# Kernel tuning notes

Measured on AMD Instinct MI355X. Metric: run time of the kernel, lower is better.

The kernel has to match this reference:

```python
import jax, jax.numpy as jnp
import numpy as np

NUM_HEAD_CHANNELS = 64
GROUPS = 32
EPS = 1e-5


def setup_inputs() -> dict:
    key = jax.random.key(0)
    ks = jax.random.split(key, 3)
    B, C, H, W = 16, 512, 64, 64
    x = jax.random.normal(ks[0], (B, C, H, W), jnp.float32)
    gn_gamma = jnp.ones((C,), jnp.float32)
    gn_beta = jnp.zeros((C,), jnp.float32)
    # 1x1 conv weights (out_ch, in_ch); fan-in scaling keeps softmax logits sane
    w_qkv = jax.random.normal(ks[1], (3 * C, C), jnp.float32) / np.float32(np.sqrt(C))
    b_qkv = jnp.zeros((3 * C,), jnp.float32)
    w_proj = jax.random.normal(ks[2], (C, C), jnp.float32) / np.float32(np.sqrt(C))
    b_proj = jnp.zeros((C,), jnp.float32)
    return dict(x=x, gn_gamma=gn_gamma, gn_beta=gn_beta, w_qkv=w_qkv,
                b_qkv=b_qkv, w_proj=w_proj, b_proj=b_proj)


def _group_norm(x, gamma, beta):
    B, C, H, W = x.shape
    xg = x.reshape(B, GROUPS, C // GROUPS, H, W)
    mu = xg.mean(axis=(2, 3, 4), keepdims=True)
    var = xg.var(axis=(2, 3, 4), keepdims=True)
    xn = ((xg - mu) * jax.lax.rsqrt(var + EPS)).reshape(B, C, H, W)
    return xn * gamma[None, :, None, None] + beta[None, :, None, None]


def reference(x, gn_gamma, gn_beta, w_qkv, b_qkv, w_proj, b_proj):
    B, C, H, W = x.shape
    L = H * W
    heads = C // NUM_HEAD_CHANNELS
    Lh = L // heads  # module splits spatial length across heads

    xn = _group_norm(x, gn_gamma, gn_beta).reshape(B, C, L)
    # 1x1 conv QKV: (3C, C) x (B, C, L) -> (B, 3C, L)
    qkv = jnp.einsum('oc,bcl->bol', w_qkv, xn) + b_qkv[None, :, None]
    qkv = qkv.reshape(B, 3 * C, heads, Lh)
    q, k, v = jnp.split(qkv, 3, axis=1)  # each (B, C, heads, Lh)

    scale = np.float32(1.0 / np.sqrt(C // heads))
    w_att = jnp.einsum('bchq,bchk->bhqk', q * scale, k)  # (B, heads, Lh, Lh)
    w_att = jax.nn.softmax(w_att.astype(jnp.float32), axis=-1).astype(q.dtype)
    a = jnp.einsum('bhqk,bchk->bchq', w_att, v)  # (B, C, heads, Lh)
    a = a.reshape(B, C, L)  # contiguous reinterpretation, as torch .view

    out = jnp.einsum('oc,bcl->bol', w_proj, a) + b_proj[None, :, None]
    return x + out.reshape(B, C, H, W)
```

## Files before the change

kernel.cpp:

```cpp
#include <hip/hip_runtime.h>

typedef unsigned short u16;
typedef __attribute__((ext_vector_type(8))) short bf16x8;
typedef __attribute__((ext_vector_type(4))) short bf16x4;
typedef __attribute__((ext_vector_type(4))) float f32x4;

__device__ __forceinline__ float bf2f(u16 u){ union { unsigned int i; float f; } v; v.i = ((unsigned int)u) << 16; return v.f; }
__device__ __forceinline__ u16 f2bf(float f){ union { float f; unsigned int i; } v; v.f = f; unsigned int r = v.i + 0x7fffu + ((v.i >> 16) & 1u); return (u16)(r >> 16); }

#define MFMA(a,b,c) __builtin_amdgcn_mfma_f32_16x16x32_bf16((a),(b),(c),0,0,0)

__device__ __forceinline__ void gl_lds16(const u16* g, u16* l){
  __builtin_amdgcn_global_load_lds((const __attribute__((address_space(1))) unsigned int*)g,
                                   (__attribute__((address_space(3))) unsigned int*)l, 16, 0, 0);
}

__global__ __launch_bounds__(256) void k_gn_stats(const float* __restrict__ x, float* __restrict__ stats){
  const int bg = blockIdx.x;
  const float4* p = (const float4*)(x + (size_t)bg * 65536);
  const int tid = threadIdx.x;
  float s = 0.f, sq = 0.f;
  for (int i = 0; i < 64; ++i){
    float4 v = p[tid + i*256];
    s += v.x + v.y + v.z + v.w;
    sq += v.x*v.x + v.y*v.y + v.z*v.z + v.w*v.w;
  }
#pragma unroll
  for (int d = 32; d > 0; d >>= 1){ s += __shfl_down(s, d, 64); sq += __shfl_down(sq, d, 64); }
  __shared__ float ls[4], lq[4];
  if ((tid & 63) == 0){ ls[tid>>6] = s; lq[tid>>6] = sq; }
  __syncthreads();
  if (tid == 0){
    float S = ls[0]+ls[1]+ls[2]+ls[3];
    float Q = lq[0]+lq[1]+lq[2]+lq[3];
    float mean = S * (1.f/65536.f);
    float var  = Q * (1.f/65536.f) - mean*mean;
    stats[bg*2]   = mean;
    stats[bg*2+1] = rsqrtf(var + 1e-5f);
  }
}

__global__ __launch_bounds__(256) void k_conv_w(const float* __restrict__ wq, const float* __restrict__ wp,
                                                u16* __restrict__ wout){
  const int base = (blockIdx.x*256 + threadIdx.x) * 4;
  float4 v;
  if (base < 786432) v = *(const float4*)(wq + base);
  else               v = *(const float4*)(wp + (base - 786432));
  bf16x4 o;
  o[0] = (short)f2bf(v.x); o[1] = (short)f2bf(v.y); o[2] = (short)f2bf(v.z); o[3] = (short)f2bf(v.w);
  *(bf16x4*)(wout + base) = o;
}

__global__ __launch_bounds__(256) void k_gn_t(const float* __restrict__ x, const float* __restrict__ stats,
                                              const float* __restrict__ gamma, const float* __restrict__ beta,
                                              u16* __restrict__ xnt){
  __shared__ u16 tile[64*72];
  const int l0 = blockIdx.x*64, c0 = blockIdx.y*64, b = blockIdx.z;
  const int tid = threadIdx.x;
#pragma unroll
  for (int i = 0; i < 2; ++i){
    int v = tid + i*256; int cc = v >> 3, seg = v & 7;
    int c = c0 + cc;
    float mu = stats[(b*32 + (c>>4))*2], rs = stats[(b*32 + (c>>4))*2 + 1];
    float ga = gamma[c] * rs;
    float be = beta[c] - mu * ga;
    const float* px = x + ((size_t)(b*512 + c))*4096 + l0 + seg*8;
    float4 a0 = *(const float4*)px;
    float4 a1 = *(const float4*)(px + 4);
    bf16x8 ov;
    ov[0]=(short)f2bf(a0.x*ga+be); ov[1]=(short)f2bf(a0.y*ga+be);
    ov[2]=(short)f2bf(a0.z*ga+be); ov[3]=(short)f2bf(a0.w*ga+be);
    ov[4]=(short)f2bf(a1.x*ga+be); ov[5]=(short)f2bf(a1.y*ga+be);
    ov[6]=(short)f2bf(a1.z*ga+be); ov[7]=(short)f2bf(a1.w*ga+be);
    *(bf16x8*)&tile[cc*72 + seg*8] = ov;
  }
  __syncthreads();
#pragma unroll
  for (int i = 0; i < 2; ++i){
    int v = tid + i*256; int ll = v >> 3, seg = v & 7;
    bf16x8 ov;
#pragma unroll
    for (int j = 0; j < 8; ++j) ov[j] = (short)tile[(seg*8 + j)*72 + ll];
    *(bf16x8*)(xnt + ((size_t)(b*4096 + l0 + ll))*512 + c0 + seg*8) = ov;
  }
}

__global__ __launch_bounds__(256,2) void k_qkv(const u16* __restrict__ xnt, const u16* __restrict__ wq,
                                               const float* __restrict__ bq,
                                               u16* __restrict__ Qt, u16* __restrict__ Kt, u16* __restrict__ Vh){
  __shared__ u16 smem[17408];
  u16* sA = smem;
  u16* sW = smem + 8192;
  const int l0 = blockIdx.x*128, o0 = blockIdx.y*128, b = blockIdx.z;
  const int tid = threadIdx.x, wv = tid>>6, lane = tid&63, g = lane>>4, r = lane&15;
  const int wm = wv>>1, wn = wv&1;
  const u16* Ab = xnt + ((size_t)(b*4096 + l0))*512;
  const u16* Wb = wq  + (size_t)o0*512;
  int srow[4], scol[4];
#pragma unroll
  for (int j = 0; j < 4; ++j){
    int s = wv*256 + j*64 + lane;
    srow[j] = s >> 3;
    scol[j] = ((s & 7) ^ (srow[j] & 7)) * 8;
  }
  f32x4 acc[4][4];
#pragma unroll
  for (int mt = 0; mt < 4; ++mt)
#pragma unroll
    for (int nt = 0; nt < 4; ++nt) acc[mt][nt] = (f32x4){0.f,0.f,0.f,0.f};

  const int key = r & 7;
  for (int c0 = 0; c0 < 512; c0 += 64){
    __syncthreads();
#pragma unroll
    for (int j = 0; j < 4; ++j){
      u16* ldst = &smem[(wv*256 + j*64)*8];
      gl_lds16(Ab + (size_t)srow[j]*512 + c0 + scol[j], ldst);
      gl_lds16(Wb + (size_t)srow[j]*512 + c0 + scol[j], ldst + 8192);
    }
    __syncthreads();
#pragma unroll
    for (int half = 0; half < 2; ++half){
      bf16x8 a[4], w[4];
#pragma unroll
      for (int mt = 0; mt < 4; ++mt){ int R = wm*64 + mt*16 + r; a[mt] = *(const bf16x8*)&sA[(R*8 + ((half*4+g) ^ key))*8]; }
#pragma unroll
      for (int nt = 0; nt < 4; ++nt){ int R = wn*64 + nt*16 + r; w[nt] = *(const bf16x8*)&sW[(R*8 + ((half*4+g) ^ key))*8]; }
#pragma unroll
      for (int mt = 0; mt < 4; ++mt)
#pragma unroll
        for (int nt = 0; nt < 4; ++nt) acc[mt][nt] = MFMA(a[mt], w[nt], acc[mt][nt]);
    }
  }
  __syncthreads();
  const int t   = blockIdx.y >> 2;
  const int cp0 = (blockIdx.y & 3)*128;
  const int h   = blockIdx.x >> 2;
  const int lh0 = (blockIdx.x & 3)*128;
#pragma unroll
  for (int nt = 0; nt < 4; ++nt){
    const int ol = wn*64 + nt*16 + r;
    const float bi = bq[o0 + ol];
#pragma unroll
    for (int mt = 0; mt < 4; ++mt){
      const int ll = wm*64 + mt*16 + g*4;
      if (t == 2){
        bf16x4 pk;
#pragma unroll
        for (int rr = 0; rr < 4; ++rr) pk[rr] = (short)f2bf(acc[mt][nt][rr] + bi);
        *(bf16x4*)&smem[ol*136 + ll] = pk;
      } else {
#pragma unroll
        for (int rr = 0; rr < 4; ++rr) smem[(ll + rr)*136 + ol] = f2bf(acc[mt][nt][rr] + bi);
      }
    }
  }
  __syncthreads();
  const size_t bh = (size_t)(b*8 + h);
  u16* dst = (t == 0) ? Qt : Kt;
#pragma unroll
  for (int i = 0; i < 8; ++i){
    int v = tid + i*256; int row = v >> 4, seg = v & 15;
    bf16x8 d = *(const bf16x8*)&smem[row*136 + seg*8];
    if (t == 2){
      *(bf16x8*)(Vh + (bh*512 + cp0 + row)*512 + lh0 + seg*8) = d;
    } else {
      *(bf16x8*)(dst + (bh*512 + lh0 + row)*512 + cp0 + seg*8) = d;
    }
  }
}

__global__ __launch_bounds__(512,2) void k_attn(const u16* __restrict__ Qt, const u16* __restrict__ Kt,
                                                const u16* __restrict__ Vh, u16* __restrict__ At){
  extern __shared__ __align__(16) u16 smem[];
  float* sMax = (float*)(smem + 65536);
  float* sSum = sMax + 512;
  const int wgid = blockIdx.x;
  const int orig = (wgid & 7)*64 + (wgid >> 3);
  const int b = orig >> 5, h = (orig >> 2) & 7, q0 = (orig & 3) * 128;
  const int bh = b*8 + h;
  const int tid = threadIdx.x, wv = tid>>6, lane = tid&63, g = lane>>4, r = lane&15;
  const int wq = wv>>2, wk = wv&3;
  const size_t base = (size_t)bh * 262144;
  const u16* Qb = Qt + base + (size_t)q0*512;
  const u16* Kb = Kt + base;
  const u16* Vb = Vh + base;

  const u16* gsrc[5];
  int ldoff[5];
  {
    const int l4 = lane >> 2, pc = lane & 3;
#pragma unroll
    for (int j = 0; j < 5; ++j){
      const int i = wv*5 + j;
      const int row = ((i < 8) ? (i*16) : ((i-8)*16)) + l4;
      const u16* bp = (i < 8) ? (Qb + (size_t)row*512) : (Kb + (size_t)row*512);
      gsrc[j] = bp + ((pc ^ (row & 3)) * 8);
      ldoff[j] = i * 512;
    }
  }

  f32x4 s[4][8];
#pragma unroll
  for (int mt = 0; mt < 4; ++mt)
#pragma unroll
    for (int nt = 0; nt < 8; ++nt) s[mt][nt] = (f32x4){0.f,0.f,0.f,0.f};

  const int qswz = (g ^ (r & 3)) * 8;

#define STAGE_QK(bufbase, c0) do { \
    u16* _bb = (bufbase); \
    _Pragma("unroll") \
    for (int _j = 0; _j < 5; ++_j) gl_lds16(gsrc[_j] + (c0), _bb + ldoff[_j]); \
  } while(0)

#define QK_COMPUTE(bbp) do { \
    const u16* _cb = (bbp); \
    bf16x8 a_[4], kb_[8]; \
    _Pragma("unroll") \
    for (int _mt = 0; _mt < 4; ++_mt) a_[_mt] = *(const bf16x8*)&_cb[(wq*64 + _mt*16 + r)*32 + qswz]; \
    _Pragma("unroll") \
    for (int _nt = 0; _nt < 8; ++_nt) kb_[_nt] = *(const bf16x8*)&_cb[4096 + (wk*128 + _nt*16 + r)*32 + qswz]; \
    __builtin_amdgcn_s_setprio(1); \
    _Pragma("unroll") \
    for (int _mt = 0; _mt < 4; ++_mt) \
      _Pragma("unroll") \
      for (int _nt = 0; _nt < 8; ++_nt) s[_mt][_nt] = MFMA(a_[_mt], kb_[_nt], s[_mt][_nt]); \
    __builtin_amdgcn_s_setprio(0); \
  } while(0)

  STAGE_QK(smem,         0);
  STAGE_QK(smem + 20480, 32);
  int bcur = 0;
  for (int cs = 0; cs < 15; ++cs){
    asm volatile("s_waitcnt vmcnt(5)" ::: "memory");
    __builtin_amdgcn_s_barrier();
    __builtin_amdgcn_sched_barrier(0);
    if (cs < 14){
      int bn = bcur + 2; if (bn >= 3) bn -= 3;
      STAGE_QK(smem + bn*20480, (cs+2)*32);
    }
    QK_COMPUTE(smem + bcur*20480);
    if (++bcur == 3) bcur = 0;
  }
  asm volatile("s_waitcnt vmcnt(0)" ::: "memory");
  __builtin_amdgcn_s_barrier();
  __builtin_amdgcn_sched_barrier(0);
  QK_COMPUTE(smem + bcur*20480);

#pragma unroll
  for (int mt = 0; mt < 4; ++mt)
#pragma unroll
    for (int nt = 0; nt < 8; ++nt)
#pragma unroll
      for (int rr = 0; rr < 4; ++rr) s[mt][nt][rr] *= 0.125f;

  float mx[4][4];
#pragma unroll
  for (int mt = 0; mt < 4; ++mt)
#pragma unroll
    for (int rr = 0; rr < 4; ++rr){
      float m = s[mt][0][rr];
#pragma unroll
      for (int nt = 1; nt < 8; ++nt) m = fmaxf(m, s[mt][nt][rr]);
      m = fmaxf(m, __shfl_xor(m, 1, 64)); m = fmaxf(m, __shfl_xor(m, 2, 64));
      m = fmaxf(m, __shfl_xor(m, 4, 64)); m = fmaxf(m, __shfl_xor(m, 8, 64));
      mx[mt][rr] = m;
    }
  if (r == 0){
#pragma unroll
    for (int mt = 0; mt < 4; ++mt)
#pragma unroll
      for (int rr = 0; rr < 4; ++rr) sMax[(wq*64 + mt*16 + g*4 + rr)*4 + wk] = mx[mt][rr];
  }
  __syncthreads();
#pragma unroll
  for (int mt = 0; mt < 4; ++mt)
#pragma unroll
    for (int rr = 0; rr < 4; ++rr){
      float4 v = *(const float4*)&sMax[(wq*64 + mt*16 + g*4 + rr)*4];
      mx[mt][rr] = fmaxf(fmaxf(v.x, v.y), fmaxf(v.z, v.w));
    }
  float inv[4][4];
#pragma unroll
  for (int mt = 0; mt < 4; ++mt)
#pragma unroll
    for (int rr = 0; rr < 4; ++rr){
      float t = 0.f;
#pragma unroll
      for (int nt = 0; nt < 8; ++nt){
        float e = __expf(s[mt][nt][rr] - mx[mt][rr]);
        s[mt][nt][rr] = e; t += e;
      }
      t += __shfl_xor(t, 1, 64); t += __shfl_xor(t, 2, 64);
      t += __shfl_xor(t, 4, 64); t += __shfl_xor(t, 8, 64);
      inv[mt][rr] = t;
    }
  if (r == 0){
#pragma unroll
    for (int mt = 0; mt < 4; ++mt)
#pragma unroll
      for (int rr = 0; rr < 4; ++rr) sSum[(wq*64 + mt*16 + g*4 + rr)*4 + wk] = inv[mt][rr];
  }
  __syncthreads();
#pragma unroll
  for (int mt = 0; mt < 4; ++mt)
#pragma unroll
    for (int rr = 0; rr < 4; ++rr){
      float4 v = *(const float4*)&sSum[(wq*64 + mt*16 + g*4 + rr)*4];
      inv[mt][rr] = 1.f / (v.x + v.y + v.z + v.w);
    }
  {
    const int kx7 = r & 7, kbase = wk*16 + (r>>3);
#pragma unroll
    for (int mt = 0; mt < 4; ++mt)
#pragma unroll
      for (int rr = 0; rr < 4; ++rr){
        const int q = wq*64 + mt*16 + g*4 + rr;
        const int ro = q*512, qx = q & 7;
        const float iv = inv[mt][rr];
#pragma unroll
        for (int nt = 0; nt < 8; ++nt){
          const int ch = kbase + nt*2;
          smem[ro + ((ch ^ qx) * 8) + kx7] = f2bf(s[mt][nt][rr] * iv);
        }
      }
  }
  const u16* Vw = Vb + (size_t)(wv*64 + r)*512 + g*8;
  bf16x8 vf[2][4];
#pragma unroll
  for (int mt = 0; mt < 4; ++mt) vf[0][mt] = *(const bf16x8*)(Vw + mt*8192);
  __syncthreads();

  f32x4 o[4][8];
#pragma unroll
  for (int mt = 0; mt < 4; ++mt)
#pragma unroll
    for (int nt = 0; nt < 8; ++nt) o[mt][nt] = (f32x4){0.f,0.f,0.f,0.f};
#pragma unroll
  for (int kk = 0; kk < 16; ++kk){
    if (kk < 15){
#pragma unroll
      for (int mt = 0; mt < 4; ++mt) vf[(kk+1)&1][mt] = *(const bf16x8*)(Vw + mt*8192 + (kk+1)*32);
    }
    bf16x8 pp[8];
#pragma unroll
    for (int nt = 0; nt < 8; ++nt){
      const int q = nt*16 + r;
      pp[nt] = *(const bf16x8*)&smem[q*512 + (((kk*4 + g) ^ (r & 7)) * 8)];
    }
    __builtin_amdgcn_s_setprio(1);
#pragma unroll
    for (int mt = 0; mt < 4; ++mt)
#pragma unroll
      for (int nt = 0; nt < 8; ++nt) o[mt][nt] = MFMA(vf[kk&1][mt], pp[nt], o[mt][nt]);
    __builtin_amdgcn_s_setprio(0);
  }
  __syncthreads();

#pragma unroll
  for (int mt = 0; mt < 4; ++mt){
    const int c = wv*64 + mt*16 + g*4;
    const int ch = c >> 3, cl = c & 7;
#pragma unroll
    for (int nt = 0; nt < 8; ++nt){
      const int q = nt*16 + r;
      bf16x4 pk;
#pragma unroll
      for (int rr = 0; rr < 4; ++rr) pk[rr] = (short)f2bf(o[mt][nt][rr]);
      *(bf16x4*)&smem[q*512 + ((ch ^ (r & 7)) * 8) + cl] = pk;
    }
  }
  __syncthreads();
  u16* Ad = At + ((size_t)(bh*512 + q0))*512;
#pragma unroll
  for (int i = 0; i < 16; ++i){
    const int idx = tid + i*512, q = idx >> 6, ch = idx & 63;
    bf16x8 d = *(const bf16x8*)&smem[q*512 + ((ch ^ (q & 7)) * 8)];
    *(bf16x8*)(Ad + (size_t)q*512 + ch*8) = d;
  }
#undef STAGE_QK
#undef QK_COMPUTE
}

__global__ __launch_bounds__(256,2) void k_proj(const u16* __restrict__ At, const u16* __restrict__ wp,
                                                const float* __restrict__ bpr, const float* __restrict__ x,
                                                float* __restrict__ out){
  __shared__ u16 smem[17408];
  u16* sA = smem;
  u16* sW = smem + 8192;
  const int l0 = blockIdx.x*128, o0 = blockIdx.y*128, b = blockIdx.z;
  const int tid = threadIdx.x, wv = tid>>6, lane = tid&63, g = lane>>4, r = lane&15;
  const int wm = wv>>1, wn = wv&1;
  const u16* Ab = At + ((size_t)(b*4096 + l0))*512;
  const u16* Wb = wp + (size_t)o0*512;
  int srow[4], scol[4];
#pragma unroll
  for (int j = 0; j < 4; ++j){
    int s = wv*256 + j*64 + lane;
    srow[j] = s >> 3;
    scol[j] = ((s & 7) ^ (srow[j] & 7)) * 8;
  }
  f32x4 acc[4][4];
#pragma unroll
  for (int mt = 0; mt < 4; ++mt)
#pragma unroll
    for (int nt = 0; nt < 4; ++nt) acc[mt][nt] = (f32x4){0.f,0.f,0.f,0.f};
  const int key = r & 7;
  for (int c0 = 0; c0 < 512; c0 += 64){
    __syncthreads();
#pragma unroll
    for (int j = 0; j < 4; ++j){
      u16* ldst = &smem[(wv*256 + j*64)*8];
      gl_lds16(Ab + (size_t)srow[j]*512 + c0 + scol[j], ldst);
      gl_lds16(Wb + (size_t)srow[j]*512 + c0 + scol[j], ldst + 8192);
    }
    __syncthreads();
#pragma unroll
    for (int half = 0; half < 2; ++half){
      bf16x8 a[4], w[4];
#pragma unroll
      for (int mt = 0; mt < 4; ++mt){ int R = wm*64 + mt*16 + r; a[mt] = *(const bf16x8*)&sA[(R*8 + ((half*4+g) ^ key))*8]; }
#pragma unroll
      for (int nt = 0; nt < 4; ++nt){ int R = wn*64 + nt*16 + r; w[nt] = *(const bf16x8*)&sW[(R*8 + ((half*4+g) ^ key))*8]; }
#pragma unroll
      for (int mt = 0; mt < 4; ++mt)
#pragma unroll
        for (int nt = 0; nt < 4; ++nt) acc[mt][nt] = MFMA(a[mt], w[nt], acc[mt][nt]);
    }
  }
  __syncthreads();
#pragma unroll
  for (int nt = 0; nt < 4; ++nt){
    const int ol = wn*64 + nt*16 + r;
    const float bi = bpr[o0 + ol];
#pragma unroll
    for (int mt = 0; mt < 4; ++mt){
      const int ll = wm*64 + mt*16 + g*4;
      bf16x4 pk;
#pragma unroll
      for (int rr = 0; rr < 4; ++rr) pk[rr] = (short)f2bf(acc[mt][nt][rr] + bi);
      *(bf16x4*)&smem[ol*136 + ll] = pk;
    }
  }
  __syncthreads();
#pragma unroll
  for (int i = 0; i < 16; ++i){
    int v = tid + i*256; int row = v >> 5, seg = v & 31;
    bf16x4 d = *(const bf16x4*)&smem[row*136 + seg*4];
    const size_t gi = ((size_t)(b*512 + o0 + row))*4096 + l0 + seg*4;
    float4 xv = *(const float4*)(x + gi);
    float4 ov;
    ov.x = bf2f((u16)d[0]) + xv.x;
    ov.y = bf2f((u16)d[1]) + xv.y;
    ov.z = bf2f((u16)d[2]) + xv.z;
    ov.w = bf2f((u16)d[3]) + xv.w;
    *(float4*)(out + gi) = ov;
  }
}

extern "C" void kernel_launch(void* const* d_in, const int* in_sizes, int n_in,
                              void* d_out, int out_size, void* d_ws, size_t ws_size,
                              hipStream_t stream) {
  (void)in_sizes; (void)n_in; (void)out_size; (void)ws_size;
  const float* x     = (const float*)d_in[0];
  const float* gamma = (const float*)d_in[1];
  const float* beta  = (const float*)d_in[2];
  const float* wqkv  = (const float*)d_in[3];
  const float* bqkv  = (const float*)d_in[4];
  const float* wproj = (const float*)d_in[5];
  const float* bproj = (const float*)d_in[6];
  float* out = (float*)d_out;
  char* ws = (char*)d_ws;

  float* stats = (float*)ws;
  u16* W16  = (u16*)(ws + 8192);
  u16* Wq16 = W16;
  u16* Wp16 = W16 + 786432;
  u16* Qt = (u16*)(ws + 8192 + 2097152);
  u16* Kt = Qt + (size_t)33554432;
  u16* Vh = Kt + (size_t)33554432;
  u16* At = Qt;
  u16* Xnt = (u16*)d_out;

  static bool attn_attr = false;
  if (!attn_attr){
    hipFuncSetAttribute((const void*)k_attn, hipFuncAttributeMaxDynamicSharedMemorySize, 135168);
    attn_attr = true;
  }

  k_gn_stats<<<512, 256, 0, stream>>>(x, stats);
  k_conv_w<<<1024, 256, 0, stream>>>(wqkv, wproj, W16);
  k_gn_t<<<dim3(64,8,16), 256, 0, stream>>>(x, stats, gamma, beta, Xnt);
  k_qkv<<<dim3(32,12,16), 256, 0, stream>>>(Xnt, Wq16, bqkv, Qt, Kt, Vh);
  k_attn<<<512, 512, 135168, stream>>>(Qt, Kt, Vh, At);
  k_proj<<<dim3(32,4,16), 256, 0, stream>>>(At, Wp16, bproj, x, out);
}
```

Baseline: 545.7 us.

## Triple-buffer K-loop with async LDS loads in QKV and projection GEMMs

Replaces the load-sync-compute K loop in the QKV and output-projection GEMMs with a three-stage ring of LDS buffers, each holding a 32-wide K chunk. Global-to-LDS loads run two stages ahead and are gated by vmcnt waits and a single barrier per step. MFMA sections are raised in priority with s_setprio, and occupancy is bumped to 3 blocks per SM. The aim is to hide global load latency behind MFMA work. The cost is a smaller K step, so there are more barriers, plus a new 4-wide swizzle and more LDS per block.

Measured after the change: 566.5 us. 3.8% more time.

```diff
diff --git a/kernel.cpp b/kernel.cpp
--- a/kernel.cpp
+++ b/kernel.cpp
@@ -85,23 +85,24 @@
   }
 }
 
-__global__ __launch_bounds__(256,2) void k_qkv(const u16* __restrict__ xnt, const u16* __restrict__ wq,
+__global__ __launch_bounds__(256,3) void k_qkv(const u16* __restrict__ xnt, const u16* __restrict__ wq,
                                                const float* __restrict__ bq,
                                                u16* __restrict__ Qt, u16* __restrict__ Kt, u16* __restrict__ Vh){
-  __shared__ u16 smem[17408];
-  u16* sA = smem;
-  u16* sW = smem + 8192;
+  __shared__ u16 smem[24576];
   const int l0 = blockIdx.x*128, o0 = blockIdx.y*128, b = blockIdx.z;
   const int tid = threadIdx.x, wv = tid>>6, lane = tid&63, g = lane>>4, r = lane&15;
   const int wm = wv>>1, wn = wv&1;
   const u16* Ab = xnt + ((size_t)(b*4096 + l0))*512;
   const u16* Wb = wq  + (size_t)o0*512;
-  int srow[4], scol[4];
+  const u16* gsrc[4];
+  int ldoff[4];
 #pragma unroll
   for (int j = 0; j < 4; ++j){
-    int s = wv*256 + j*64 + lane;
-    srow[j] = s >> 3;
-    scol[j] = ((s & 7) ^ (srow[j] & 7)) * 8;
+    const int s = j*256 + tid;
+    const int row = s >> 2, pc = s & 3;
+    const int lc = pc ^ (row & 3);
+    gsrc[j] = ((row < 128) ? (Ab + (size_t)row*512) : (Wb + (size_t)(row - 128)*512)) + lc*8;
+    ldoff[j] = (j*256 + wv*64)*8;
   }
   f32x4 acc[4][4];
 #pragma unroll
@@ -109,29 +110,52 @@
 #pragma unroll
     for (int nt = 0; nt < 4; ++nt) acc[mt][nt] = (f32x4){0.f,0.f,0.f,0.f};
 
-  const int key = r & 7;
-  for (int c0 = 0; c0 < 512; c0 += 64){
-    __syncthreads();
-#pragma unroll
-    for (int j = 0; j < 4; ++j){
-      u16* ldst = &smem[(wv*256 + j*64)*8];
-      gl_lds16(Ab + (size_t)srow[j]*512 + c0 + scol[j], ldst);
-      gl_lds16(Wb + (size_t)srow[j]*512 + c0 + scol[j], ldst + 8192);
-    }
-    __syncthreads();
-#pragma unroll
-    for (int half = 0; half < 2; ++half){
-      bf16x8 a[4], w[4];
-#pragma unroll
-      for (int mt = 0; mt < 4; ++mt){ int R = wm*64 + mt*16 + r; a[mt] = *(const bf16x8*)&sA[(R*8 + ((half*4+g) ^ key))*8]; }
-#pragma unroll
-      for (int nt = 0; nt < 4; ++nt){ int R = wn*64 + nt*16 + r; w[nt] = *(const bf16x8*)&sW[(R*8 + ((half*4+g) ^ key))*8]; }
-#pragma unroll
-      for (int mt = 0; mt < 4; ++mt)
-#pragma unroll
-        for (int nt = 0; nt < 4; ++nt) acc[mt][nt] = MFMA(a[mt], w[nt], acc[mt][nt]);
-    }
-  }
+#define STG3(bufo, c0) do { \
+    u16* _bb = smem + (bufo); \
+    _Pragma("unroll") \
+    for (int _j = 0; _j < 4; ++_j) gl_lds16(gsrc[_j] + (c0), _bb + ldoff[_j]); \
+  } while(0)
+
+#define CMP3(bufo) do { \
+    const u16* _cb = smem + (bufo); \
+    const int _sw = (g ^ (r & 3)) * 8; \
+    bf16x8 a_[4], w_[4]; \
+    _Pragma("unroll") \
+    for (int _mt = 0; _mt < 4; ++_mt) a_[_mt] = *(const bf16x8*)&_cb[(wm*64 + _mt*16 + r)*32 + _sw]; \
+    _Pragma("unroll") \
+    for (int _nt = 0; _nt < 4; ++_nt) w_[_nt] = *(const bf16x8*)&_cb[4096 + (wn*64 + _nt*16 + r)*32 + _sw]; \
+    __builtin_amdgcn_s_setprio(1); \
+    _Pragma("unroll") \
+    for (int _mt = 0; _mt < 4; ++_mt) \
+      _Pragma("unroll") \
+      for (int _nt = 0; _nt < 4; ++_nt) acc[_mt][_nt] = MFMA(a_[_mt], w_[_nt], acc[_mt][_nt]); \
+    __builtin_amdgcn_s_setprio(0); \
+  } while(0)
+
+  STG3(0,     0);
+  STG3(8192, 32);
+  int cur = 0;
+  for (int cs = 0; cs < 14; ++cs){
+    asm volatile("s_waitcnt vmcnt(4)" ::: "memory");
+    __builtin_amdgcn_s_barrier();
+    __builtin_amdgcn_sched_barrier(0);
+    int bn = cur + 2; if (bn >= 3) bn -= 3;
+    STG3(bn*8192, (cs + 2)*32);
+    CMP3(cur*8192);
+    if (++cur == 3) cur = 0;
+  }
+  asm volatile("s_waitcnt vmcnt(4)" ::: "memory");
+  __builtin_amdgcn_s_barrier();
+  __builtin_amdgcn_sched_barrier(0);
+  CMP3(cur*8192);
+  if (++cur == 3) cur = 0;
+  asm volatile("s_waitcnt vmcnt(0)" ::: "memory");
+  __builtin_amdgcn_s_barrier();
+  __builtin_amdgcn_sched_barrier(0);
+  CMP3(cur*8192);
+#undef STG3
+#undef CMP3
+
   __syncthreads();
   const int t   = blockIdx.y >> 2;
   const int cp0 = (blockIdx.y & 3)*128;
@@ -383,52 +407,77 @@
 #undef QK_COMPUTE
 }
 
-__global__ __launch_bounds__(256,2) void k_proj(const u16* __restrict__ At, const u16* __restrict__ wp,
+__global__ __launch_bounds__(256,3) void k_proj(const u16* __restrict__ At, const u16* __restrict__ wp,
                                                 const float* __restrict__ bpr, const float* __restrict__ x,
                                                 float* __restrict__ out){
-  __shared__ u16 smem[17408];
-  u16* sA = smem;
-  u16* sW = smem + 8192;
+  __shared__ u16 smem[24576];
   const int l0 = blockIdx.x*128, o0 = blockIdx.y*128, b = blockIdx.z;
   const int tid = threadIdx.x, wv = tid>>6, lane = tid&63, g = lane>>4, r = lane&15;
   const int wm = wv>>1, wn = wv&1;
   const u16* Ab = At + ((size_t)(b*4096 + l0))*512;
   const u16* Wb = wp + (size_t)o0*512;
-  int srow[4], scol[4];
+  const u16* gsrc[4];
+  int ldoff[4];
 #pragma unroll
   for (int j = 0; j < 4; ++j){
-    int s = wv*256 + j*64 + lane;
-    srow[j] = s >> 3;
-    scol[j] = ((s & 7) ^ (srow[j] & 7)) * 8;
+    const int s = j*256 + tid;
+    const int row = s >> 2, pc = s & 3;
+    const int lc = pc ^ (row & 3);
+    gsrc[j] = ((row < 128) ? (Ab + (size_t)row*512) : (Wb + (size_t)(row - 128)*512)) + lc*8;
+    ldoff[j] = (j*256 + wv*64)*8;
   }
   f32x4 acc[4][4];
 #pragma unroll
   for (int mt = 0; mt < 4; ++mt)
 #pragma unroll
     for (int nt = 0; nt < 4; ++nt) acc[mt][nt] = (f32x4){0.f,0.f,0.f,0.f};
-  const int key = r & 7;
-  for (int c0 = 0; c0 < 512; c0 += 64){
-    __syncthreads();
-#pragma unroll
-    for (int j = 0; j < 4; ++j){
-      u16* ldst = &smem[(wv*256 + j*64)*8];
-      gl_lds16(Ab + (size_t)srow[j]*512 + c0 + scol[j], ldst);
-      gl_lds16(Wb + (size_t)srow[j]*512 + c0 + scol[j], ldst + 8192);
-    }
-    __syncthreads();
-#pragma unroll
-    for (int half = 0; half < 2; ++half){
-      bf16x8 a[4], w[4];
-#pragma unroll
-      for (int mt = 0; mt < 4; ++mt){ int R = wm*64 + mt*16 + r; a[mt] = *(const bf16x8*)&sA[(R*8 + ((half*4+g) ^ key))*8]; }
-#pragma unroll
-      for (int nt = 0; nt < 4; ++nt){ int R = wn*64 + nt*16 + r; w[nt] = *(const bf16x8*)&sW[(R*8 + ((half*4+g) ^ key))*8]; }
-#pragma unroll
-      for (int mt = 0; mt < 4; ++mt)
-#pragma unroll
-        for (int nt = 0; nt < 4; ++nt) acc[mt][nt] = MFMA(a[mt], w[nt], acc[mt][nt]);
-    }
-  }
+
+#define STG5(bufo, c0) do { \
+    u16* _bb = smem + (bufo); \
+    _Pragma("unroll") \
+    for (int _j = 0; _j < 4; ++_j) gl_lds16(gsrc[_j] + (c0), _bb + ldoff[_j]); \
+  } while(0)
+
+#define CMP5(bufo) do { \
+    const u16* _cb = smem + (bufo); \
+    const int _sw = (g ^ (r & 3)) * 8; \
+    bf16x8 a_[4], w_[4]; \
+    _Pragma("unroll") \
+    for (int _mt = 0; _mt < 4; ++_mt) a_[_mt] = *(const bf16x8*)&_cb[(wm*64 + _mt*16 + r)*32 + _sw]; \
+    _Pragma("unroll") \
+    for (int _nt = 0; _nt < 4; ++_nt) w_[_nt] = *(const bf16x8*)&_cb[4096 + (wn*64 + _nt*16 + r)*32 + _sw]; \
+    __builtin_amdgcn_s_setprio(1); \
+    _Pragma("unroll") \
+    for (int _mt = 0; _mt < 4; ++_mt) \
+      _Pragma("unroll") \
+      for (int _nt = 0; _nt < 4; ++_nt) acc[_mt][_nt] = MFMA(a_[_mt], w_[_nt], acc[_mt][_nt]); \
+    __builtin_amdgcn_s_setprio(0); \
+  } while(0)
+
+  STG5(0,     0);
+  STG5(8192, 32);
+  int cur = 0;
+  for (int cs = 0; cs < 14; ++cs){
+    asm volatile("s_waitcnt vmcnt(4)" ::: "memory");
+    __builtin_amdgcn_s_barrier();
+    __builtin_amdgcn_sched_barrier(0);
+    int bn = cur + 2; if (bn >= 3) bn -= 3;
+    STG5(bn*8192, (cs + 2)*32);
+    CMP5(cur*8192);
+    if (++cur == 3) cur = 0;
+  }
+  asm volatile("s_waitcnt vmcnt(4)" ::: "memory");
+  __builtin_amdgcn_s_barrier();
+  __builtin_amdgcn_sched_barrier(0);
+  CMP5(cur*8192);
+  if (++cur == 3) cur = 0;
+  asm volatile("s_waitcnt vmcnt(0)" ::: "memory");
+  __builtin_amdgcn_s_barrier();
+  __builtin_amdgcn_sched_barrier(0);
+  CMP5(cur*8192);
+#undef STG5
+#undef CMP5
+
   __syncthreads();
 #pragma unroll
   for (int nt = 0; nt < 4; ++nt){
```

## Rewrite QKV GEMM with 256x256 tiles and double-buffered async LDS pipeline

Applied to the files above, without the earlier changes.

The QKV projection kernel now uses 512-thread blocks that compute 256x256 output tiles, with double-buffered 128KB dynamic LDS. Global-to-LDS loads for the next K-chunk are issued while MFMAs run on the current one, coordinated by explicit barriers and waitcnt. The LDS swizzle changes to a 4-chunk pattern keyed on row>>1, and the attention kernel's swizzle is updated to match. The aim is to cut global traffic through larger reuse and to hide load latency, at the cost of higher register and LDS pressure and a two-pass epilogue.

Result: slower. 581.0 us (+6.5%).

```diff
diff --git a/kernel.cpp b/kernel.cpp
--- a/kernel.cpp
+++ b/kernel.cpp
@@ -85,87 +85,169 @@
   }
 }
 
-__global__ __launch_bounds__(256,2) void k_qkv(const u16* __restrict__ xnt, const u16* __restrict__ wq,
+__global__ __launch_bounds__(512,2) void k_qkv(const u16* __restrict__ xnt, const u16* __restrict__ wq,
                                                const float* __restrict__ bq,
                                                u16* __restrict__ Qt, u16* __restrict__ Kt, u16* __restrict__ Vh){
-  __shared__ u16 smem[17408];
-  u16* sA = smem;
-  u16* sW = smem + 8192;
-  const int l0 = blockIdx.x*128, o0 = blockIdx.y*128, b = blockIdx.z;
+  extern __shared__ __align__(16) u16 smem[];
+  const int l0 = blockIdx.x*256, o0 = blockIdx.y*256, b = blockIdx.z;
   const int tid = threadIdx.x, wv = tid>>6, lane = tid&63, g = lane>>4, r = lane&15;
-  const int wm = wv>>1, wn = wv&1;
+  const int wm = wv>>2, wn = wv&3;
   const u16* Ab = xnt + ((size_t)(b*4096 + l0))*512;
   const u16* Wb = wq  + (size_t)o0*512;
-  int srow[4], scol[4];
-#pragma unroll
-  for (int j = 0; j < 4; ++j){
-    int s = wv*256 + j*64 + lane;
-    srow[j] = s >> 3;
-    scol[j] = ((s & 7) ^ (srow[j] & 7)) * 8;
-  }
-  f32x4 acc[4][4];
-#pragma unroll
-  for (int mt = 0; mt < 4; ++mt)
+  const u16 *Asrc[2], *Wsrc[2];
+  int ldo[2];
+#pragma unroll
+  for (int j = 0; j < 2; ++j){
+    const int cid = j*512 + tid;
+    const int row = cid >> 2, pc = cid & 3;
+    const int lc = pc ^ ((row >> 1) & 3);
+    Asrc[j] = Ab + (size_t)row*512 + lc*8;
+    Wsrc[j] = Wb + (size_t)row*512 + lc*8;
+    ldo[j] = (j*512 + wv*64)*8;
+  }
+  f32x4 acc[8][4];
+#pragma unroll
+  for (int mt = 0; mt < 8; ++mt)
 #pragma unroll
     for (int nt = 0; nt < 4; ++nt) acc[mt][nt] = (f32x4){0.f,0.f,0.f,0.f};
-
-  const int key = r & 7;
-  for (int c0 = 0; c0 < 512; c0 += 64){
-    __syncthreads();
-#pragma unroll
-    for (int j = 0; j < 4; ++j){
-      u16* ldst = &smem[(wv*256 + j*64)*8];
-      gl_lds16(Ab + (size_t)srow[j]*512 + c0 + scol[j], ldst);
-      gl_lds16(Wb + (size_t)srow[j]*512 + c0 + scol[j], ldst + 8192);
-    }
-    __syncthreads();
-#pragma unroll
-    for (int half = 0; half < 2; ++half){
-      bf16x8 a[4], w[4];
-#pragma unroll
-      for (int mt = 0; mt < 4; ++mt){ int R = wm*64 + mt*16 + r; a[mt] = *(const bf16x8*)&sA[(R*8 + ((half*4+g) ^ key))*8]; }
-#pragma unroll
-      for (int nt = 0; nt < 4; ++nt){ int R = wn*64 + nt*16 + r; w[nt] = *(const bf16x8*)&sW[(R*8 + ((half*4+g) ^ key))*8]; }
-#pragma unroll
-      for (int mt = 0; mt < 4; ++mt)
-#pragma unroll
-        for (int nt = 0; nt < 4; ++nt) acc[mt][nt] = MFMA(a[mt], w[nt], acc[mt][nt]);
-    }
-  }
-  __syncthreads();
-  const int t   = blockIdx.y >> 2;
-  const int cp0 = (blockIdx.y & 3)*128;
-  const int h   = blockIdx.x >> 2;
-  const int lh0 = (blockIdx.x & 3)*128;
-#pragma unroll
-  for (int nt = 0; nt < 4; ++nt){
-    const int ol = wn*64 + nt*16 + r;
-    const float bi = bq[o0 + ol];
-#pragma unroll
-    for (int mt = 0; mt < 4; ++mt){
-      const int ll = wm*64 + mt*16 + g*4;
-      if (t == 2){
-        bf16x4 pk;
-#pragma unroll
-        for (int rr = 0; rr < 4; ++rr) pk[rr] = (short)f2bf(acc[mt][nt][rr] + bi);
-        *(bf16x4*)&smem[ol*136 + ll] = pk;
-      } else {
-#pragma unroll
-        for (int rr = 0; rr < 4; ++rr) smem[(ll + rr)*136 + ol] = f2bf(acc[mt][nt][rr] + bi);
+  const int key = (r >> 1) & 3;
+
+#define STGU(regionu16, srcarr, koff) do { \
+    u16* _d = smem + (regionu16); \
+    _Pragma("unroll") \
+    for (int _j = 0; _j < 2; ++_j) gl_lds16(srcarr[_j] + (koff), _d + ldo[_j]); \
+  } while(0)
+#define LDA(kk, mo) do { \
+    _Pragma("unroll") \
+    for (int _i = 0; _i < 4; ++_i) \
+      a_[_i] = *(const bf16x8*)&smem[c + (kk)*8192 + ((wm*128 + ((mo)+_i)*16 + r)*4 + (g ^ key))*8]; \
+  } while(0)
+#define LDW(kk) do { \
+    _Pragma("unroll") \
+    for (int _i = 0; _i < 4; ++_i) \
+      w_[_i] = *(const bf16x8*)&smem[c + 16384 + (kk)*8192 + ((wn*64 + _i*16 + r)*4 + (g ^ key))*8]; \
+  } while(0)
+#define MM(mo) do { \
+    __builtin_amdgcn_s_setprio(1); \
+    _Pragma("unroll") \
+    for (int _i = 0; _i < 4; ++_i) \
+      _Pragma("unroll") \
+      for (int _j = 0; _j < 4; ++_j) acc[(mo)+_i][_j] = MFMA(a_[_i], w_[_j], acc[(mo)+_i][_j]); \
+    __builtin_amdgcn_s_setprio(0); \
+  } while(0)
+#define BAR()   do { __builtin_amdgcn_s_barrier(); __builtin_amdgcn_sched_barrier(0); } while(0)
+#define LGKM0() do { asm volatile("s_waitcnt lgkmcnt(0)" ::: "memory"); __builtin_amdgcn_sched_barrier(0); } while(0)
+
+  STGU(0,     Asrc, 0);
+  STGU(16384, Wsrc, 0);
+  STGU(8192,  Asrc, 32);
+  STGU(24576, Wsrc, 32);
+  asm volatile("s_waitcnt vmcnt(4)" ::: "memory");
+  BAR();
+
+  for (int t = 0; t < 7; ++t){
+    const int c  = (t & 1) << 15;
+    const int nb = c ^ 32768;
+    const int ko = (t + 1) * 64;
+    bf16x8 a_[4], w_[4];
+    LDA(0, 0); LDW(0);
+    STGU(nb,         Asrc, ko);
+    BAR(); LGKM0();
+    MM(0);
+    BAR();
+    LDA(0, 4);
+    STGU(nb + 16384, Wsrc, ko);
+    BAR(); LGKM0();
+    MM(4);
+    asm volatile("s_waitcnt vmcnt(4)" ::: "memory");
+    BAR();
+    LDA(1, 0); LDW(1);
+    STGU(nb + 8192,  Asrc, ko + 32);
+    BAR(); LGKM0();
+    MM(0);
+    BAR();
+    LDA(1, 4);
+    STGU(nb + 24576, Wsrc, ko + 32);
+    BAR(); LGKM0();
+    MM(4);
+    asm volatile("s_waitcnt vmcnt(4)" ::: "memory");
+    BAR();
+  }
+  {
+    const int c = 32768;
+    bf16x8 a_[4], w_[4];
+    LDA(0, 0); LDW(0); BAR(); LGKM0(); MM(0); BAR();
+    LDA(0, 4);         BAR(); LGKM0(); MM(4);
+    asm volatile("s_waitcnt vmcnt(0)" ::: "memory");
+    BAR();
+    LDA(1, 0); LDW(1); BAR(); LGKM0(); MM(0); BAR();
+    LDA(1, 4);         BAR(); LGKM0(); MM(4);
+  }
+#undef STGU
+#undef LDA
+#undef LDW
+#undef MM
+#undef BAR
+#undef LGKM0
+
+  __syncthreads();
+  const int t   = blockIdx.y >> 1;
+  const int cp0 = (blockIdx.y & 1)*256;
+  const int h   = blockIdx.x >> 1;
+  const int lh0 = (blockIdx.x & 1)*256;
+  const size_t bh = (size_t)(b*8 + h);
+  if (t < 2){
+    u16* dst = (t == 0) ? Qt : Kt;
+#pragma unroll
+    for (int p = 0; p < 2; ++p){
+      if (wm == p){
+#pragma unroll
+        for (int nt = 0; nt < 4; ++nt){
+          const int ol = wn*64 + nt*16 + r;
+          const float bi = bq[o0 + ol];
+#pragma unroll
+          for (int mt = 0; mt < 8; ++mt){
+            const int ll = mt*16 + g*4;
+#pragma unroll
+            for (int rr = 0; rr < 4; ++rr) smem[(ll + rr)*264 + ol] = f2bf(acc[mt][nt][rr] + bi);
+          }
+        }
       }
-    }
-  }
-  __syncthreads();
-  const size_t bh = (size_t)(b*8 + h);
-  u16* dst = (t == 0) ? Qt : Kt;
-#pragma unroll
-  for (int i = 0; i < 8; ++i){
-    int v = tid + i*256; int row = v >> 4, seg = v & 15;
-    bf16x8 d = *(const bf16x8*)&smem[row*136 + seg*8];
-    if (t == 2){
-      *(bf16x8*)(Vh + (bh*512 + cp0 + row)*512 + lh0 + seg*8) = d;
-    } else {
-      *(bf16x8*)(dst + (bh*512 + lh0 + row)*512 + cp0 + seg*8) = d;
+      __syncthreads();
+#pragma unroll
+      for (int i = 0; i < 8; ++i){
+        int v = i*512 + tid; int row = v >> 5, seg = v & 31;
+        bf16x8 d = *(const bf16x8*)&smem[row*264 + seg*8];
+        *(bf16x8*)(dst + (bh*512 + lh0 + p*128 + row)*512 + cp0 + seg*8) = d;
+      }
+      __syncthreads();
+    }
+  } else {
+#pragma unroll
+    for (int p = 0; p < 2; ++p){
+      if ((wn >> 1) == p){
+#pragma unroll
+        for (int nt = 0; nt < 4; ++nt){
+          const int ol = (wn & 1)*64 + nt*16 + r;
+          const float bi = bq[o0 + p*128 + ol];
+#pragma unroll
+          for (int mt = 0; mt < 8; ++mt){
+            const int ll = wm*128 + mt*16 + g*4;
+            bf16x4 pk;
+#pragma unroll
+            for (int rr = 0; rr < 4; ++rr) pk[rr] = (short)f2bf(acc[mt][nt][rr] + bi);
+            *(bf16x4*)&smem[ol*264 + ll] = pk;
+          }
+        }
+      }
+      __syncthreads();
+#pragma unroll
+      for (int i = 0; i < 8; ++i){
+        int v = i*512 + tid; int row = v >> 5, seg = v & 31;
+        bf16x8 d = *(const bf16x8*)&smem[row*264 + seg*8];
+        *(bf16x8*)(Vh + (bh*512 + cp0 + p*128 + row)*512 + lh0 + seg*8) = d;
+      }
+      __syncthreads();
     }
   }
 }
@@ -195,7 +277,7 @@
       const int i = wv*5 + j;
       const int row = ((i < 8) ? (i*16) : ((i-8)*16)) + l4;
       const u16* bp = (i < 8) ? (Qb + (size_t)row*512) : (Kb + (size_t)row*512);
-      gsrc[j] = bp + ((pc ^ (row & 3)) * 8);
+      gsrc[j] = bp + ((pc ^ ((row >> 1) & 3)) * 8);
       ldoff[j] = i * 512;
     }
   }
@@ -206,7 +288,7 @@
 #pragma unroll
     for (int nt = 0; nt < 8; ++nt) s[mt][nt] = (f32x4){0.f,0.f,0.f,0.f};
 
-  const int qswz = (g ^ (r & 3)) * 8;
+  const int qswz = (g ^ ((r >> 1) & 3)) * 8;
 
 #define STAGE_QK(bufbase, c0) do { \
     u16* _bb = (bufbase); \
@@ -486,13 +568,14 @@
   static bool attn_attr = false;
   if (!attn_attr){
     hipFuncSetAttribute((const void*)k_attn, hipFuncAttributeMaxDynamicSharedMemorySize, 135168);
+    hipFuncSetAttribute((const void*)k_qkv,  hipFuncAttributeMaxDynamicSharedMemorySize, 131072);
     attn_attr = true;
   }
 
   k_gn_stats<<<512, 256, 0, stream>>>(x, stats);
   k_conv_w<<<1024, 256, 0, stream>>>(wqkv, wproj, W16);
   k_gn_t<<<dim3(64,8,16), 256, 0, stream>>>(x, stats, gamma, beta, Xnt);
-  k_qkv<<<dim3(32,12,16), 256, 0, stream>>>(Xnt, Wq16, bqkv, Qt, Kt, Vh);
+  k_qkv<<<dim3(16,6,16), 512, 131072, stream>>>(Xnt, Wq16, bqkv, Qt, Kt, Vh);
   k_attn<<<512, 512, 135168, stream>>>(Qt, Kt, Vh, At);
   k_proj<<<dim3(32,4,16), 256, 0, stream>>>(At, Wp16, bproj, x, out);
 }
```
